# Kernel optimization log

Hardware: AMD Instinct MI355X
Metric: run time of the kernel (lower is better)

The kernel has to match this reference:

```python
import jax, jax.numpy as jnp
import numpy as np

B = 256
NUM_PRIMARY = 32      # cfg.num_primary_caps
PRIM_ATOMS = 8
NUM_CLASSES = 10
DIGIT_ATOMS = 16
NUM_ROUTING = 3       # cfg.num_routing (DigitCap)
IN_DIM = 6 * 6 * NUM_PRIMARY  # 1152
NUM_PIXELS = 28 * 28 * 1


def squash(s, axis):
    # v = ||s||^2/(1+||s||^2) * s/||s||
    n2 = jnp.sum(jnp.square(s), axis=axis, keepdims=True)
    return s * (n2 / (1.0 + n2)) / jnp.sqrt(n2 + 1e-9)


def conv2d(x, w, stride):
    return jax.lax.conv_general_dilated(
        x, w, (stride, stride), 'VALID',
        dimension_numbers=('NCHW', 'OIHW', 'NCHW'))


def setup_inputs() -> dict:
    key = jax.random.key(0)
    ks = jax.random.split(key, 10)
    x = jax.random.uniform(ks[0], (B, 1, 28, 28), jnp.float32)
    labels = jax.random.randint(ks[1], (B,), 0, NUM_CLASSES)
    y = jax.nn.one_hot(labels, NUM_CLASSES, dtype=jnp.float32)
    conv1_w = 0.05 * jax.random.normal(ks[2], (256, 1, 9, 9), jnp.float32)
    conv1_b = jnp.full((256,), 0.1, jnp.float32)
    # primary capsule conv: 256 -> 32 caps * 8 atoms, k=9, s=2 (bias applied after routing)
    prim_w = 0.05 * jax.random.normal(ks[3], (NUM_PRIMARY * PRIM_ATOMS, 256, 9, 9), jnp.float32)
    prim_b = jnp.full((NUM_PRIMARY, PRIM_ATOMS), 0.1, jnp.float32)
    # digit capsule transform: [in_dim, in_atoms, out_dim, out_atoms]
    digit_w = 0.05 * jax.random.normal(ks[4], (IN_DIM, PRIM_ATOMS, NUM_CLASSES, DIGIT_ATOMS), jnp.float32)
    digit_b = jnp.full((NUM_CLASSES, DIGIT_ATOMS), 0.1, jnp.float32)
    w1 = 0.05 * jax.random.normal(ks[5], (NUM_CLASSES * DIGIT_ATOMS, 512), jnp.float32)
    b1 = jnp.zeros((512,), jnp.float32)
    w2 = 0.05 * jax.random.normal(ks[6], (512, 1024), jnp.float32)
    b2 = jnp.zeros((1024,), jnp.float32)
    w3 = 0.05 * jax.random.normal(ks[7], (1024, NUM_PIXELS), jnp.float32)
    b3 = jnp.zeros((NUM_PIXELS,), jnp.float32)
    return dict(x=x, y=y, conv1_w=conv1_w, conv1_b=conv1_b, prim_w=prim_w,
                prim_b=prim_b, digit_w=digit_w, digit_b=digit_b,
                w1=w1, b1=b1, w2=w2, b2=b2, w3=w3, b3=b3)


def reference(x, y, conv1_w, conv1_b, prim_w, prim_b, digit_w, digit_b,
              w1, b1, w2, b2, w3, b3):
    # conv stem
    h = jax.nn.relu(conv2d(x, conv1_w, 1) + conv1_b[None, :, None, None])  # [B,256,20,20]

    # PrimaryCap: conv votes [B, in_dim=1, out=32, atoms=8, 6, 6]; num_routing=1
    votes_p = conv2d(h, prim_w, 2).reshape(B, NUM_PRIMARY, PRIM_ATOMS, 6, 6)
    # one routing iter, input_dim=1: softmax(zeros) over output_dim -> uniform 1/32
    preact_p = votes_p / NUM_PRIMARY + prim_b[None, :, :, None, None]
    caps1 = squash(preact_p, axis=2)  # [B,32,8,6,6]

    # permute(0,1,3,4,2) then flatten -> [B, 1152, 8]
    x3 = jnp.transpose(caps1, (0, 1, 3, 4, 2)).reshape(B, IN_DIM, PRIM_ATOMS)

    # DigitCap votes: [B, in_dim, out_dim, out_atoms]
    votes = jnp.einsum('bia,iaot->biot', x3, digit_w)
    logits = jnp.zeros((B, IN_DIM, NUM_CLASSES), votes.dtype)
    act = None
    for _ in range(NUM_ROUTING):
        route = jax.nn.softmax(logits, axis=2)  # over output capsules
        preact = jnp.einsum('bio,biot->bot', route, votes) + digit_b
        act = squash(preact, axis=-1)  # [B,10,16]
        logits = logits + jnp.einsum('biot,bot->bio', votes, act)
    digit = act

    # Reconstruction: mask by label, 160 -> 512 -> 1024 -> 784
    masked = (digit * y[:, :, None]).reshape(B, NUM_CLASSES * DIGIT_ATOMS)
    r = jax.nn.relu(masked @ w1 + b1)
    r = jax.nn.relu(r @ w2 + b2)
    recon = jax.nn.sigmoid(r @ w3 + b3)
    return digit, recon
```

## Files before the change

### kernel.cpp

```cpp
#include <hip/hip_runtime.h>
#include <hip/hip_bf16.h>

typedef unsigned short u16;
typedef unsigned int u32;

static __device__ __forceinline__ float us2f(u16 u) {
    return __uint_as_float(((u32)u) << 16);
}
static __device__ __forceinline__ u16 f2bu(float f) {
    u32 u = __float_as_uint(f);
    return (u16)((u + 0x7fffu + ((u >> 16) & 1u)) >> 16);
}

typedef __attribute__((ext_vector_type(8))) __bf16 bf16x8;
typedef __attribute__((ext_vector_type(4))) float f32x4;

__global__ void fill_sentinel(float* out, int n, float val) {
    int g = blockIdx.x * 256 + threadIdx.x;
    if (g < n) out[g] = val;
}

__global__ __launch_bounds__(256) void conv_c1wb(const float* __restrict__ w,
                                                 u16* __restrict__ wb)
{
    const int j = blockIdx.x, c = threadIdx.x;
    wb[j * 256 + c] = f2bu(w[c * 81 + j]);
}

__global__ __launch_bounds__(256) void conv1_kernel(const float* __restrict__ x,
    const u16* __restrict__ wb, const float* __restrict__ bias, u16* __restrict__ h)
{
    __shared__ float xs[784];
    __shared__ u16 wl[81 * 256];
    const int b = blockIdx.x >> 2, g = blockIdx.x & 3;
    const int c = threadIdx.x;
    for (int idx = c; idx < 784; idx += 256) xs[idx] = x[b * 784 + idx];
    for (int idx = c; idx < 20736; idx += 256) wl[idx] = wb[idx];
    __syncthreads();
    const float bv = bias[c];
    #pragma unroll 1
    for (int iy = g * 5; iy < g * 5 + 5; ++iy) {
        float acc[20];
        #pragma unroll
        for (int i = 0; i < 20; ++i) acc[i] = bv;
        #pragma unroll 1
        for (int dy = 0; dy < 9; ++dy) {
            float xr[28];
            const float4* xrow = reinterpret_cast<const float4*>(&xs[(iy + dy) * 28]);
            #pragma unroll
            for (int i = 0; i < 7; ++i) {
                float4 v = xrow[i];
                xr[4*i] = v.x; xr[4*i+1] = v.y; xr[4*i+2] = v.z; xr[4*i+3] = v.w;
            }
            #pragma unroll
            for (int dx = 0; dx < 9; ++dx) {
                const float wv = us2f(wl[(dy * 9 + dx) * 256 + c]);
                #pragma unroll
                for (int ix = 0; ix < 20; ++ix) acc[ix] += xr[ix + dx] * wv;
            }
        }
        u16* hp = h + ((b * 20 + iy) * 20) * 256 + c;
        #pragma unroll
        for (int ix = 0; ix < 20; ++ix) hp[ix * 256] = f2bu(fmaxf(acc[ix], 0.f));
    }
}

__global__ __launch_bounds__(256) void transpose_primw(const float* __restrict__ w,
                                                       u16* __restrict__ wt)
{
    __shared__ u16 wl[81 * 258];
    const int n = blockIdx.x, tid = threadIdx.x;
    const float* ws = w + (size_t)n * 20736;
    for (int idx = tid; idx < 20736; idx += 256) {
        const int cc = idx / 81, kk = idx - cc * 81;
        wl[kk * 258 + cc] = f2bu(ws[idx]);
    }
    __syncthreads();
    u16* wo = wt + (size_t)n * 20736;
    for (int q = tid; q < 20736; q += 256)
        wo[q] = wl[(q >> 8) * 258 + (q & 255)];
}

__global__ __launch_bounds__(256) void conv_dwb(const float* __restrict__ dw,
    u16* __restrict__ dwb_t, u16* __restrict__ dwb_a)
{
    const int g = blockIdx.x * 256 + threadIdx.x;
    const float v = dw[g];
    const u16 bv = f2bu(v);
    dwb_t[g] = bv;
    const int i = g / 1280, rem = g % 1280;
    const int a = rem / 160, ot = rem % 160;
    dwb_a[((size_t)i * 160 + ot) * 8 + a] = bv;
}

__global__ __launch_bounds__(256) void prim_gemm_split(const u16* __restrict__ h,
    const u16* __restrict__ wT, float* __restrict__ pm)
{
    __shared__ u16 As[128 * 40];
    __shared__ u16 Bs[128 * 40];
    const int tid = threadIdx.x;
    const int split = blockIdx.y;
    const int mt = blockIdx.x % 72, nt = blockIdx.x / 72;
    const int mBase = mt * 128, nBase = nt * 128;
    const int tq = tid & 3, tr = tid >> 2;
    int m0 = mBase + tr;
    int b0 = m0 / 36, r0 = m0 % 36;
    int aBase0 = ((b0 * 20 + 2 * (r0 / 6)) * 20 + 2 * (r0 % 6)) * 256 + tq * 8;
    int m1 = m0 + 64;
    int b1 = m1 / 36, r1 = m1 % 36;
    int aBase1 = ((b1 * 20 + 2 * (r1 / 6)) * 20 + 2 * (r1 % 6)) * 256 + tq * 8;
    const int bBase0 = (nBase + tr) * 20736 + tq * 8;
    const int bBase1 = (nBase + tr + 64) * 20736 + tq * 8;
    int kglob = split * 1728;
    int ky = kglob / 2304; int krem = kglob - ky * 2304;
    int kx = krem >> 8; int c0 = krem & 255;

    f32x4 acc[4][4];
    #pragma unroll
    for (int i = 0; i < 4; ++i)
        #pragma unroll
        for (int j = 0; j < 4; ++j) acc[i][j] = (f32x4){0.f, 0.f, 0.f, 0.f};

    const int lane = tid & 63;
    const int wvi = tid >> 6; const int wm = wvi >> 1, wn = wvi & 1;
    const int lcol = lane & 15, lquad = lane >> 4;
    const u16* Arow = As + (wm * 64 + lcol) * 40 + lquad * 8;
    const u16* Brow = Bs + (wn * 64 + lcol) * 40 + lquad * 8;

    #pragma unroll 1
    for (int kt = 0; kt < 54; ++kt) {
        const int koffA = (ky * 20 + kx) * 256 + c0;
        uint4 ra0 = *reinterpret_cast<const uint4*>(h + aBase0 + koffA);
        uint4 ra1 = *reinterpret_cast<const uint4*>(h + aBase1 + koffA);
        uint4 rb0 = *reinterpret_cast<const uint4*>(wT + bBase0 + kglob);
        uint4 rb1 = *reinterpret_cast<const uint4*>(wT + bBase1 + kglob);
        __syncthreads();
        *reinterpret_cast<uint4*>(As + tr * 40 + tq * 8)        = ra0;
        *reinterpret_cast<uint4*>(As + (tr + 64) * 40 + tq * 8) = ra1;
        *reinterpret_cast<uint4*>(Bs + tr * 40 + tq * 8)        = rb0;
        *reinterpret_cast<uint4*>(Bs + (tr + 64) * 40 + tq * 8) = rb1;
        __syncthreads();
        bf16x8 af[4], bfr[4];
        #pragma unroll
        for (int i = 0; i < 4; ++i)
            af[i] = *reinterpret_cast<const bf16x8*>(Arow + i * 640);
        #pragma unroll
        for (int j = 0; j < 4; ++j)
            bfr[j] = *reinterpret_cast<const bf16x8*>(Brow + j * 640);
        #pragma unroll
        for (int i = 0; i < 4; ++i)
            #pragma unroll
            for (int j = 0; j < 4; ++j)
                acc[i][j] = __builtin_amdgcn_mfma_f32_16x16x32_bf16(af[i], bfr[j], acc[i][j], 0, 0, 0);
        kglob += 32; c0 += 32;
        if (c0 == 256) { c0 = 0; if (++kx == 9) { kx = 0; ++ky; } }
    }
    #pragma unroll
    for (int i = 0; i < 4; ++i) {
        const int mrow = mBase + wm * 64 + i * 16 + lquad * 4;
        #pragma unroll
        for (int j = 0; j < 4; ++j) {
            const int ncol = nBase + wn * 64 + j * 16 + lcol;
            #pragma unroll
            for (int r = 0; r < 4; ++r)
                unsafeAtomicAdd(&pm[(size_t)(mrow + r) * 256 + ncol], acc[i][j][r]);
        }
    }
}

__global__ __launch_bounds__(256) void squash_kernel(float* __restrict__ pm,
    const float* __restrict__ pb)
{
    const int m = blockIdx.x, t = threadIdx.x;
    float pre = pm[(size_t)m * 256 + t] * (1.f / 32.f) + pb[t];
    float sq = pre * pre;
    sq += __shfl_xor(sq, 1); sq += __shfl_xor(sq, 2); sq += __shfl_xor(sq, 4);
    float scale = (sq / (1.f + sq)) * rsqrtf(sq + 1e-9f);
    pm[(size_t)m * 256 + t] = pre * scale;
}

__global__ __launch_bounds__(256) void routing_act_part(const float* __restrict__ x3m,
    const u16* __restrict__ dwb_a, const float* __restrict__ logits,
    float* __restrict__ preactD, int uniform)
{
    __shared__ float x3s[8192];
    __shared__ float rs[10240];
    const int c = blockIdx.x, bg = blockIdx.y;
    const int tid = threadIdx.x;
    for (int q = tid; q < 8192; q += 256) {
        const int b_l = q >> 10, rest = q & 1023, il = rest >> 3, a = rest & 7;
        const int i = c * 128 + il, cap = i / 36, p = i - cap * 36;
        x3s[q] = x3m[((size_t)(bg * 8 + b_l) * 36 + p) * 256 + cap * 8 + a];
    }
    if (!uniform && tid < 128) {
        const int i = c * 128 + tid;
        for (int b_l = 0; b_l < 8; ++b_l) {
            const float* lg = &logits[((size_t)(bg * 8 + b_l) * 1152 + i) * 10];
            float l[10]; float mx = -1e30f;
            #pragma unroll
            for (int k = 0; k < 10; ++k) { l[k] = lg[k]; mx = fmaxf(mx, l[k]); }
            float s = 0.f;
            #pragma unroll
            for (int k = 0; k < 10; ++k) { l[k] = __expf(l[k] - mx); s += l[k]; }
            const float inv = 1.f / s;
            #pragma unroll
            for (int k = 0; k < 10; ++k) rs[(b_l * 128 + tid) * 10 + k] = l[k] * inv;
        }
    }
    __syncthreads();
    if (tid < 160) {
        const int ot = tid;
        const int o = tid >> 4;
        float preg[8];
        #pragma unroll
        for (int b_l = 0; b_l < 8; ++b_l) preg[b_l] = 0.f;
        #pragma unroll 2
        for (int il = 0; il < 128; ++il) {
            const int i = c * 128 + il;
            const uint4 dq = *reinterpret_cast<const uint4*>(
                &dwb_a[((size_t)i * 160 + ot) * 8]);
            const u32 du[4] = {dq.x, dq.y, dq.z, dq.w};
            float dv[8];
            #pragma unroll
            for (int q = 0; q < 4; ++q) {
                dv[2 * q]     = __uint_as_float(du[q] << 16);
                dv[2 * q + 1] = __uint_as_float(du[q] & 0xffff0000u);
            }
            #pragma unroll
            for (int b_l = 0; b_l < 8; ++b_l) {
                const float* xp = &x3s[(b_l * 128 + il) * 8];
                float v = 0.f;
                #pragma unroll
                for (int a = 0; a < 8; ++a) v += xp[a] * dv[a];
                const float r = uniform ? 0.1f : rs[(b_l * 128 + il) * 10 + o];
                preg[b_l] += r * v;
            }
        }
        #pragma unroll
        for (int b_l = 0; b_l < 8; ++b_l)
            unsafeAtomicAdd(&preactD[(size_t)(bg * 8 + b_l) * 160 + tid], preg[b_l]);
    }
}

__global__ __launch_bounds__(192) void routing_squash(const float* __restrict__ preactD,
    const float* __restrict__ db, float* __restrict__ act, float* __restrict__ dout)
{
    const int b = blockIdx.x, tid = threadIdx.x;
    if (tid < 160) {
        float pre = preactD[(size_t)b * 160 + tid] + db[tid];
        float sq = pre * pre;
        sq += __shfl_xor(sq, 1); sq += __shfl_xor(sq, 2);
        sq += __shfl_xor(sq, 4); sq += __shfl_xor(sq, 8);
        float scale = (sq / (1.f + sq)) * rsqrtf(sq + 1e-9f);
        float a = pre * scale;
        act[(size_t)b * 160 + tid] = a;
        if (dout) dout[(size_t)b * 160 + tid] = a;
    }
}

__global__ __launch_bounds__(256) void routing_upd_part(const float* __restrict__ x3m,
    const u16* __restrict__ dwb_t, const float* __restrict__ act,
    float* __restrict__ logits, int first)
{
    __shared__ float x3s[8192];
    __shared__ float acts[1280];
    const int c = blockIdx.x, bg = blockIdx.y;
    const int tid = threadIdx.x;
    for (int q = tid; q < 8192; q += 256) {
        const int b_l = q >> 10, rest = q & 1023, il = rest >> 3, a = rest & 7;
        const int i = c * 128 + il, cap = i / 36, p = i - cap * 36;
        x3s[q] = x3m[((size_t)(bg * 8 + b_l) * 36 + p) * 256 + cap * 8 + a];
    }
    for (int q = tid; q < 1280; q += 256)
        acts[q] = act[(size_t)(bg * 8 + q / 160) * 160 + (q % 160)];
    __syncthreads();
    const int il = tid >> 1, half = tid & 1;
    const int i = c * 128 + il;
    #pragma unroll 1
    for (int oo = 0; oo < 5; ++oo) {
        const int o = half * 5 + oo;
        float s[8];
        #pragma unroll
        for (int b_l = 0; b_l < 8; ++b_l) s[b_l] = 0.f;
        #pragma unroll
        for (int a = 0; a < 8; ++a) {
            const uint4* dp = reinterpret_cast<const uint4*>(
                &dwb_t[(((size_t)i * 8 + a) * 10 + o) * 16]);
            uint4 d0 = dp[0], d1 = dp[1];
            const u32 du[8] = {d0.x, d0.y, d0.z, d0.w, d1.x, d1.y, d1.z, d1.w};
            #pragma unroll
            for (int b_l = 0; b_l < 8; ++b_l) {
                const float* ap = &acts[b_l * 160 + o * 16];
                float inner = 0.f;
                #pragma unroll
                for (int q = 0; q < 8; ++q) {
                    inner += __uint_as_float(du[q] << 16) * ap[2 * q];
                    inner += __uint_as_float(du[q] & 0xffff0000u) * ap[2 * q + 1];
                }
                s[b_l] += x3s[(b_l * 128 + il) * 8 + a] * inner;
            }
        }
        #pragma unroll
        for (int b_l = 0; b_l < 8; ++b_l) {
            float* lp = &logits[((size_t)(bg * 8 + b_l) * 1152 + i) * 10 + o];
            if (first) *lp = s[b_l]; else *lp += s[b_l];
        }
    }
}

__global__ __launch_bounds__(256) void masked_kernel(const float* __restrict__ act,
    const float* __restrict__ y, float* __restrict__ masked)
{
    const int gid = blockIdx.x * 256 + threadIdx.x;
    const int b = gid / 160, j = gid % 160;
    masked[gid] = act[gid] * y[b * 10 + (j >> 4)];
}

__global__ __launch_bounds__(256) void mlp_layer(const float* __restrict__ in,
    const float* __restrict__ w, const float* __restrict__ bias,
    float* __restrict__ outp, int K, int N, int mode)
{
    __shared__ float ins[2 * 1024];
    const int b0 = blockIdx.x * 2;
    const int n = blockIdx.y * 256 + threadIdx.x;
    for (int idx = threadIdx.x; idx < 2 * K; idx += 256)
        ins[idx] = in[(size_t)b0 * K + idx];
    __syncthreads();
    if (n < N) {
        float a0 = 0.f, a1 = 0.f;
        for (int k = 0; k < K; ++k) {
            const float wvv = w[(size_t)k * N + n];
            a0 += ins[k] * wvv;
            a1 += ins[K + k] * wvv;
        }
        const float bv = bias[n];
        float v[2] = {a0 + bv, a1 + bv};
        #pragma unroll
        for (int j = 0; j < 2; ++j) {
            float xv = v[j];
            xv = (mode == 0) ? fmaxf(xv, 0.f) : 1.f / (1.f + __expf(-xv));
            outp[(size_t)(b0 + j) * N + n] = xv;
        }
    }
}

extern "C" void kernel_launch(void* const* d_in, const int* in_sizes, int n_in,
                              void* d_out, int out_size, void* d_ws, size_t ws_size,
                              hipStream_t stream) {
    const float* x   = (const float*)d_in[0];
    const float* y   = (const float*)d_in[1];
    const float* c1w = (const float*)d_in[2];
    const float* c1b = (const float*)d_in[3];
    const float* pw  = (const float*)d_in[4];
    const float* pb  = (const float*)d_in[5];
    const float* dw  = (const float*)d_in[6];
    const float* db  = (const float*)d_in[7];
    const float* w1  = (const float*)d_in[8];
    const float* b1  = (const float*)d_in[9];
    const float* w2  = (const float*)d_in[10];
    const float* b2  = (const float*)d_in[11];
    const float* w3  = (const float*)d_in[12];
    const float* b3  = (const float*)d_in[13];
    float* out = (float*)d_out;
    char* ws = (char*)d_ws;

    static const int exp_sizes[14] = {200704, 2560, 20736, 256, 5308416, 256,
                                      1474560, 160, 81920, 512, 524288, 1024,
                                      802816, 784};
    int bad = (n_in == 14) ? -1 : -2;
    if (bad == -1)
        for (int i = 0; i < 14; ++i) if (in_sizes[i] != exp_sizes[i]) { bad = i; break; }
    if (bad != -1) {
        fill_sentinel<<<(out_size + 255) / 256, 256, 0, stream>>>(out, out_size,
            7168.f + 16.f * (float)(bad + 1));
        return;
    }
    const size_t NEEDED = 72482816ULL;
    if (ws_size < NEEDED) {
        fill_sentinel<<<(out_size + 255) / 256, 256, 0, stream>>>(out, out_size, 111.0f);
        return;
    }

    u16*   h       = (u16*)(ws);
    u16*   wT2     = (u16*)(ws + 52428800);
    float* x3m     = (float*)(ws + 63045632);
    u16*   c1wb    = (u16*)(ws + 63045632);
    float* logits  = (float*)(ws);
    float* act     = (float*)(ws + 11796480);
    float* masked  = (float*)(ws + 11960320);
    float* r1      = (float*)(ws + 12124160);
    float* r2      = (float*)(ws + 12648448);
    float* preactD = (float*)(ws + 13697024);
    u16*   dwb_t   = (u16*)(ws + 13860864);
    u16*   dwb_a   = (u16*)(ws + 16809984);

    conv_c1wb<<<81, 256, 0, stream>>>(c1w, c1wb);
    conv1_kernel<<<1024, 256, 0, stream>>>(x, c1wb, c1b, h);
    transpose_primw<<<256, 256, 0, stream>>>(pw, wT2);
    hipMemsetAsync(x3m, 0, 9437184, stream);
    prim_gemm_split<<<dim3(144, 12), 256, 0, stream>>>(h, wT2, x3m);
    squash_kernel<<<9216, 256, 0, stream>>>(x3m, pb);
    conv_dwb<<<5760, 256, 0, stream>>>(dw, dwb_t, dwb_a);

    hipMemsetAsync(preactD, 0, 163840, stream);
    routing_act_part<<<dim3(9, 32), 256, 0, stream>>>(x3m, dwb_a, logits, preactD, 1);
    routing_squash<<<256, 192, 0, stream>>>(preactD, db, act, (float*)nullptr);
    routing_upd_part<<<dim3(9, 32), 256, 0, stream>>>(x3m, dwb_t, act, logits, 1);

    hipMemsetAsync(preactD, 0, 163840, stream);
    routing_act_part<<<dim3(9, 32), 256, 0, stream>>>(x3m, dwb_a, logits, preactD, 0);
    routing_squash<<<256, 192, 0, stream>>>(preactD, db, act, (float*)nullptr);
    routing_upd_part<<<dim3(9, 32), 256, 0, stream>>>(x3m, dwb_t, act, logits, 0);

    hipMemsetAsync(preactD, 0, 163840, stream);
    routing_act_part<<<dim3(9, 32), 256, 0, stream>>>(x3m, dwb_a, logits, preactD, 0);
    routing_squash<<<256, 192, 0, stream>>>(preactD, db, act, out);

    masked_kernel<<<160, 256, 0, stream>>>(act, y, masked);
    mlp_layer<<<dim3(128, 2), 256, 0, stream>>>(masked, w1, b1, r1, 160, 512, 0);
    mlp_layer<<<dim3(128, 4), 256, 0, stream>>>(r1, w2, b2, r2, 512, 1024, 0);
    mlp_layer<<<dim3(128, 4), 256, 0, stream>>>(r2, w3, b3, out + 40960, 1024, 784, 1);
}
```

Before: 813.1 us.

## Drop LDS from primary GEMM, halve routing tiles, fuse mask into MLP

The primary-capsule GEMM now loads MFMA fragments directly from global memory into registers, with a one-step register prefetch. It also drops the LDS staging and both barriers, and uses 8 K-splits instead of 12, so fewer atomics. Routing kernels process 64 input capsules per block instead of 128, doubling the grid, and the three preactivation memsets are merged into one using separate buffers. The masking kernel is folded into the first MLP layer, and the MLP kernels now handle four batch rows per block. Direct global fragment loads are uncoalesced and rely on cache reuse, which may hurt bandwidth.

New measurement: 1.156 ms. 1.42x slower.

```diff
diff --git a/kernel.cpp b/kernel.cpp
--- a/kernel.cpp
+++ b/kernel.cpp
@@ -93,27 +93,32 @@
     dwb_a[((size_t)i * 160 + ot) * 8 + a] = bv;
 }
 
-__global__ __launch_bounds__(256) void prim_gemm_split(const u16* __restrict__ h,
+__global__ __launch_bounds__(256) void prim_gemm_noLDS(const u16* __restrict__ h,
     const u16* __restrict__ wT, float* __restrict__ pm)
 {
-    __shared__ u16 As[128 * 40];
-    __shared__ u16 Bs[128 * 40];
     const int tid = threadIdx.x;
     const int split = blockIdx.y;
     const int mt = blockIdx.x % 72, nt = blockIdx.x / 72;
     const int mBase = mt * 128, nBase = nt * 128;
-    const int tq = tid & 3, tr = tid >> 2;
-    int m0 = mBase + tr;
-    int b0 = m0 / 36, r0 = m0 % 36;
-    int aBase0 = ((b0 * 20 + 2 * (r0 / 6)) * 20 + 2 * (r0 % 6)) * 256 + tq * 8;
-    int m1 = m0 + 64;
-    int b1 = m1 / 36, r1 = m1 % 36;
-    int aBase1 = ((b1 * 20 + 2 * (r1 / 6)) * 20 + 2 * (r1 % 6)) * 256 + tq * 8;
-    const int bBase0 = (nBase + tr) * 20736 + tq * 8;
-    const int bBase1 = (nBase + tr + 64) * 20736 + tq * 8;
-    int kglob = split * 1728;
+    const int lane = tid & 63;
+    const int wvi = tid >> 6, wm = wvi >> 1, wn = wvi & 1;
+    const int lcol = lane & 15, lquad = lane >> 4;
+
+    int aBase[4];
+    #pragma unroll
+    for (int i = 0; i < 4; ++i) {
+        const int m = mBase + wm * 64 + i * 16 + lcol;
+        const int bb = m / 36, r = m % 36;
+        aBase[i] = ((bb * 20 + 2 * (r / 6)) * 20 + 2 * (r % 6)) * 256 + lquad * 8;
+    }
+    size_t bBase[4];
+    #pragma unroll
+    for (int j = 0; j < 4; ++j)
+        bBase[j] = (size_t)(nBase + wn * 64 + j * 16 + lcol) * 20736 + lquad * 8;
+
+    int kglob = split * 2592;
     int ky = kglob / 2304; int krem = kglob - ky * 2304;
-    int kx = krem >> 8; int c0 = krem & 255;
+    int kx = krem >> 8, c0 = krem & 255;
 
     f32x4 acc[4][4];
     #pragma unroll
@@ -121,40 +126,43 @@
         #pragma unroll
         for (int j = 0; j < 4; ++j) acc[i][j] = (f32x4){0.f, 0.f, 0.f, 0.f};
 
-    const int lane = tid & 63;
-    const int wvi = tid >> 6; const int wm = wvi >> 1, wn = wvi & 1;
-    const int lcol = lane & 15, lquad = lane >> 4;
-    const u16* Arow = As + (wm * 64 + lcol) * 40 + lquad * 8;
-    const u16* Brow = Bs + (wn * 64 + lcol) * 40 + lquad * 8;
+    bf16x8 af0[4], bf0[4];
+    {
+        const int koffA = (ky * 20 + kx) * 256 + c0;
+        #pragma unroll
+        for (int i = 0; i < 4; ++i)
+            af0[i] = *reinterpret_cast<const bf16x8*>(h + aBase[i] + koffA);
+        #pragma unroll
+        for (int j = 0; j < 4; ++j)
+            bf0[j] = *reinterpret_cast<const bf16x8*>(wT + bBase[j] + kglob);
+    }
 
     #pragma unroll 1
-    for (int kt = 0; kt < 54; ++kt) {
-        const int koffA = (ky * 20 + kx) * 256 + c0;
-        uint4 ra0 = *reinterpret_cast<const uint4*>(h + aBase0 + koffA);
-        uint4 ra1 = *reinterpret_cast<const uint4*>(h + aBase1 + koffA);
-        uint4 rb0 = *reinterpret_cast<const uint4*>(wT + bBase0 + kglob);
-        uint4 rb1 = *reinterpret_cast<const uint4*>(wT + bBase1 + kglob);
-        __syncthreads();
-        *reinterpret_cast<uint4*>(As + tr * 40 + tq * 8)        = ra0;
-        *reinterpret_cast<uint4*>(As + (tr + 64) * 40 + tq * 8) = ra1;
-        *reinterpret_cast<uint4*>(Bs + tr * 40 + tq * 8)        = rb0;
-        *reinterpret_cast<uint4*>(Bs + (tr + 64) * 40 + tq * 8) = rb1;
-        __syncthreads();
-        bf16x8 af[4], bfr[4];
-        #pragma unroll
-        for (int i = 0; i < 4; ++i)
-            af[i] = *reinterpret_cast<const bf16x8*>(Arow + i * 640);
-        #pragma unroll
-        for (int j = 0; j < 4; ++j)
-            bfr[j] = *reinterpret_cast<const bf16x8*>(Brow + j * 640);
-        #pragma unroll
-        for (int i = 0; i < 4; ++i)
-            #pragma unroll
-            for (int j = 0; j < 4; ++j)
-                acc[i][j] = __builtin_amdgcn_mfma_f32_16x16x32_bf16(af[i], bfr[j], acc[i][j], 0, 0, 0);
+    for (int kt = 0; kt < 80; ++kt) {
         kglob += 32; c0 += 32;
         if (c0 == 256) { c0 = 0; if (++kx == 9) { kx = 0; ++ky; } }
-    }
+        const int koffA = (ky * 20 + kx) * 256 + c0;
+        bf16x8 af1[4], bf1[4];
+        #pragma unroll
+        for (int i = 0; i < 4; ++i)
+            af1[i] = *reinterpret_cast<const bf16x8*>(h + aBase[i] + koffA);
+        #pragma unroll
+        for (int j = 0; j < 4; ++j)
+            bf1[j] = *reinterpret_cast<const bf16x8*>(wT + bBase[j] + kglob);
+        #pragma unroll
+        for (int i = 0; i < 4; ++i)
+            #pragma unroll
+            for (int j = 0; j < 4; ++j)
+                acc[i][j] = __builtin_amdgcn_mfma_f32_16x16x32_bf16(af0[i], bf0[j], acc[i][j], 0, 0, 0);
+        #pragma unroll
+        for (int i = 0; i < 4; ++i) { af0[i] = af1[i]; bf0[i] = bf1[i]; }
+    }
+    #pragma unroll
+    for (int i = 0; i < 4; ++i)
+        #pragma unroll
+        for (int j = 0; j < 4; ++j)
+            acc[i][j] = __builtin_amdgcn_mfma_f32_16x16x32_bf16(af0[i], bf0[j], acc[i][j], 0, 0, 0);
+
     #pragma unroll
     for (int i = 0; i < 4; ++i) {
         const int mrow = mBase + wm * 64 + i * 16 + lquad * 4;
@@ -183,18 +191,19 @@
     const u16* __restrict__ dwb_a, const float* __restrict__ logits,
     float* __restrict__ preactD, int uniform)
 {
-    __shared__ float x3s[8192];
-    __shared__ float rs[10240];
+    __shared__ float x3s[4096];
+    __shared__ float rs[5120];
     const int c = blockIdx.x, bg = blockIdx.y;
     const int tid = threadIdx.x;
-    for (int q = tid; q < 8192; q += 256) {
-        const int b_l = q >> 10, rest = q & 1023, il = rest >> 3, a = rest & 7;
-        const int i = c * 128 + il, cap = i / 36, p = i - cap * 36;
+    for (int q = tid; q < 4096; q += 256) {
+        const int b_l = q >> 9, rest = q & 511, il = rest >> 3, a = rest & 7;
+        const int i = c * 64 + il, cap = i / 36, p = i - cap * 36;
         x3s[q] = x3m[((size_t)(bg * 8 + b_l) * 36 + p) * 256 + cap * 8 + a];
     }
-    if (!uniform && tid < 128) {
-        const int i = c * 128 + tid;
-        for (int b_l = 0; b_l < 8; ++b_l) {
+    if (!uniform) {
+        for (int q = tid; q < 512; q += 256) {
+            const int b_l = q >> 6, il = q & 63;
+            const int i = c * 64 + il;
             const float* lg = &logits[((size_t)(bg * 8 + b_l) * 1152 + i) * 10];
             float l[10]; float mx = -1e30f;
             #pragma unroll
@@ -204,19 +213,18 @@
             for (int k = 0; k < 10; ++k) { l[k] = __expf(l[k] - mx); s += l[k]; }
             const float inv = 1.f / s;
             #pragma unroll
-            for (int k = 0; k < 10; ++k) rs[(b_l * 128 + tid) * 10 + k] = l[k] * inv;
+            for (int k = 0; k < 10; ++k) rs[(b_l * 64 + il) * 10 + k] = l[k] * inv;
         }
     }
     __syncthreads();
     if (tid < 160) {
-        const int ot = tid;
-        const int o = tid >> 4;
+        const int ot = tid, o = tid >> 4;
         float preg[8];
         #pragma unroll
         for (int b_l = 0; b_l < 8; ++b_l) preg[b_l] = 0.f;
-        #pragma unroll 2
-        for (int il = 0; il < 128; ++il) {
-            const int i = c * 128 + il;
+        #pragma unroll 4
+        for (int il = 0; il < 64; ++il) {
+            const int i = c * 64 + il;
             const uint4 dq = *reinterpret_cast<const uint4*>(
                 &dwb_a[((size_t)i * 160 + ot) * 8]);
             const u32 du[4] = {dq.x, dq.y, dq.z, dq.w};
@@ -228,11 +236,11 @@
             }
             #pragma unroll
             for (int b_l = 0; b_l < 8; ++b_l) {
-                const float* xp = &x3s[(b_l * 128 + il) * 8];
+                const float* xp = &x3s[(b_l * 64 + il) * 8];
                 float v = 0.f;
                 #pragma unroll
                 for (int a = 0; a < 8; ++a) v += xp[a] * dv[a];
-                const float r = uniform ? 0.1f : rs[(b_l * 128 + il) * 10 + o];
+                const float r = uniform ? 0.1f : rs[(b_l * 64 + il) * 10 + o];
                 preg[b_l] += r * v;
             }
         }
@@ -258,24 +266,24 @@
     }
 }
 
-__global__ __launch_bounds__(256) void routing_upd_part(const float* __restrict__ x3m,
+__global__ __launch_bounds__(128) void routing_upd_part(const float* __restrict__ x3m,
     const u16* __restrict__ dwb_t, const float* __restrict__ act,
     float* __restrict__ logits, int first)
 {
-    __shared__ float x3s[8192];
+    __shared__ float x3s[4096];
     __shared__ float acts[1280];
     const int c = blockIdx.x, bg = blockIdx.y;
     const int tid = threadIdx.x;
-    for (int q = tid; q < 8192; q += 256) {
-        const int b_l = q >> 10, rest = q & 1023, il = rest >> 3, a = rest & 7;
-        const int i = c * 128 + il, cap = i / 36, p = i - cap * 36;
+    for (int q = tid; q < 4096; q += 128) {
+        const int b_l = q >> 9, rest = q & 511, il = rest >> 3, a = rest & 7;
+        const int i = c * 64 + il, cap = i / 36, p = i - cap * 36;
         x3s[q] = x3m[((size_t)(bg * 8 + b_l) * 36 + p) * 256 + cap * 8 + a];
     }
-    for (int q = tid; q < 1280; q += 256)
+    for (int q = tid; q < 1280; q += 128)
         acts[q] = act[(size_t)(bg * 8 + q / 160) * 160 + (q % 160)];
     __syncthreads();
     const int il = tid >> 1, half = tid & 1;
-    const int i = c * 128 + il;
+    const int i = c * 64 + il;
     #pragma unroll 1
     for (int oo = 0; oo < 5; ++oo) {
         const int o = half * 5 + oo;
@@ -297,7 +305,7 @@
                     inner += __uint_as_float(du[q] << 16) * ap[2 * q];
                     inner += __uint_as_float(du[q] & 0xffff0000u) * ap[2 * q + 1];
                 }
-                s[b_l] += x3s[(b_l * 128 + il) * 8 + a] * inner;
+                s[b_l] += x3s[(b_l * 64 + il) * 8 + a] * inner;
             }
         }
         #pragma unroll
@@ -308,35 +316,35 @@
     }
 }
 
-__global__ __launch_bounds__(256) void masked_kernel(const float* __restrict__ act,
-    const float* __restrict__ y, float* __restrict__ masked)
-{
-    const int gid = blockIdx.x * 256 + threadIdx.x;
-    const int b = gid / 160, j = gid % 160;
-    masked[gid] = act[gid] * y[b * 10 + (j >> 4)];
-}
-
 __global__ __launch_bounds__(256) void mlp_layer(const float* __restrict__ in,
-    const float* __restrict__ w, const float* __restrict__ bias,
-    float* __restrict__ outp, int K, int N, int mode)
-{
-    __shared__ float ins[2 * 1024];
-    const int b0 = blockIdx.x * 2;
+    const float* __restrict__ maskY, const float* __restrict__ w,
+    const float* __restrict__ bias, float* __restrict__ outp, int K, int N, int mode)
+{
+    __shared__ float ins[4 * 1024];
+    const int b0 = blockIdx.x * 4;
     const int n = blockIdx.y * 256 + threadIdx.x;
-    for (int idx = threadIdx.x; idx < 2 * K; idx += 256)
-        ins[idx] = in[(size_t)b0 * K + idx];
+    for (int idx = threadIdx.x; idx < 4 * K; idx += 256) {
+        float v = in[(size_t)b0 * K + idx];
+        if (maskY) {
+            const int b_l = idx / K, j = idx % K;
+            v *= maskY[(b0 + b_l) * 10 + (j >> 4)];
+        }
+        ins[idx] = v;
+    }
     __syncthreads();
     if (n < N) {
-        float a0 = 0.f, a1 = 0.f;
+        float a0 = 0.f, a1 = 0.f, a2 = 0.f, a3 = 0.f;
         for (int k = 0; k < K; ++k) {
             const float wvv = w[(size_t)k * N + n];
             a0 += ins[k] * wvv;
             a1 += ins[K + k] * wvv;
+            a2 += ins[2 * K + k] * wvv;
+            a3 += ins[3 * K + k] * wvv;
         }
         const float bv = bias[n];
-        float v[2] = {a0 + bv, a1 + bv};
-        #pragma unroll
-        for (int j = 0; j < 2; ++j) {
+        float v[4] = {a0 + bv, a1 + bv, a2 + bv, a3 + bv};
+        #pragma unroll
+        for (int j = 0; j < 4; ++j) {
             float xv = v[j];
             xv = (mode == 0) ? fmaxf(xv, 0.f) : 1.f / (1.f + __expf(-xv));
             outp[(size_t)(b0 + j) * N + n] = xv;
@@ -387,37 +395,34 @@
     u16*   c1wb    = (u16*)(ws + 63045632);
     float* logits  = (float*)(ws);
     float* act     = (float*)(ws + 11796480);
-    float* masked  = (float*)(ws + 11960320);
-    float* r1      = (float*)(ws + 12124160);
-    float* r2      = (float*)(ws + 12648448);
-    float* preactD = (float*)(ws + 13697024);
-    u16*   dwb_t   = (u16*)(ws + 13860864);
-    u16*   dwb_a   = (u16*)(ws + 16809984);
+    float* r1      = (float*)(ws + 11960320);
+    float* r2      = (float*)(ws + 12484608);
+    float* preactD = (float*)(ws + 13533184);
+    u16*   dwb_t   = (u16*)(ws + 14024704);
+    u16*   dwb_a   = (u16*)(ws + 16973824);
 
     conv_c1wb<<<81, 256, 0, stream>>>(c1w, c1wb);
     conv1_kernel<<<1024, 256, 0, stream>>>(x, c1wb, c1b, h);
     transpose_primw<<<256, 256, 0, stream>>>(pw, wT2);
     hipMemsetAsync(x3m, 0, 9437184, stream);
-    prim_gemm_split<<<dim3(144, 12), 256, 0, stream>>>(h, wT2, x3m);
+    prim_gemm_noLDS<<<dim3(144, 8), 256, 0, stream>>>(h, wT2, x3m);
     squash_kernel<<<9216, 256, 0, stream>>>(x3m, pb);
     conv_dwb<<<5760, 256, 0, stream>>>(dw, dwb_t, dwb_a);
-
-    hipMemsetAsync(preactD, 0, 163840, stream);
-    routing_act_part<<<dim3(9, 32), 256, 0, stream>>>(x3m, dwb_a, logits, preactD, 1);
-    routing_squash<<<256, 192, 0, stream>>>(preactD, db, act, (float*)nullptr);
-    routing_upd_part<<<dim3(9, 32), 256, 0, stream>>>(x3m, dwb_t, act, logits, 1);
-
-    hipMemsetAsync(preactD, 0, 163840, stream);
-    routing_act_part<<<dim3(9, 32), 256, 0, stream>>>(x3m, dwb_a, logits, preactD, 0);
-    routing_squash<<<256, 192, 0, stream>>>(preactD, db, act, (float*)nullptr);
-    routing_upd_part<<<dim3(9, 32), 256, 0, stream>>>(x3m, dwb_t, act, logits, 0);
-
-    hipMemsetAsync(preactD, 0, 163840, stream);
-    routing_act_part<<<dim3(9, 32), 256, 0, stream>>>(x3m, dwb_a, logits, preactD, 0);
-    routing_squash<<<256, 192, 0, stream>>>(preactD, db, act, out);
-
-    masked_kernel<<<160, 256, 0, stream>>>(act, y, masked);
-    mlp_layer<<<dim3(128, 2), 256, 0, stream>>>(masked, w1, b1, r1, 160, 512, 0);
-    mlp_layer<<<dim3(128, 4), 256, 0, stream>>>(r1, w2, b2, r2, 512, 1024, 0);
-    mlp_layer<<<dim3(128, 4), 256, 0, stream>>>(r2, w3, b3, out + 40960, 1024, 784, 1);
-}
+    hipMemsetAsync(preactD, 0, 491520, stream);
+
+    float* pD0 = preactD, *pD1 = preactD + 40960, *pD2 = preactD + 81920;
+    routing_act_part<<<dim3(18, 32), 256, 0, stream>>>(x3m, dwb_a, logits, pD0, 1);
+    routing_squash<<<256, 192, 0, stream>>>(pD0, db, act, (float*)nullptr);
+    routing_upd_part<<<dim3(18, 32), 128, 0, stream>>>(x3m, dwb_t, act, logits, 1);
+
+    routing_act_part<<<dim3(18, 32), 256, 0, stream>>>(x3m, dwb_a, logits, pD1, 0);
+    routing_squash<<<256, 192, 0, stream>>>(pD1, db, act, (float*)nullptr);
+    routing_upd_part<<<dim3(18, 32), 128, 0, stream>>>(x3m, dwb_t, act, logits, 0);
+
+    routing_act_part<<<dim3(18, 32), 256, 0, stream>>>(x3m, dwb_a, logits, pD2, 0);
+    routing_squash<<<256, 192, 0, stream>>>(pD2, db, act, out);
+
+    mlp_layer<<<dim3(64, 2), 256, 0, stream>>>(act, y, w1, b1, r1, 160, 512, 0);
+    mlp_layer<<<dim3(64, 4), 256, 0, stream>>>(r1, (float*)nullptr, w2, b2, r2, 512, 1024, 0);
+    mlp_layer<<<dim3(64, 4), 256, 0, stream>>>(r2, (float*)nullptr, w3, b3, out + 40960, 1024, 784, 1);
+}
```
